# Performance work log

Measured on AMD Instinct MI355X. Metric: run time of the kernel, lower is better.

Reference implementation:

```python
import jax, jax.numpy as jnp
import numpy as np

N = 50000   # nodes
E = 640000  # edges
D_IN = 128
D_OUT = 128
EPS = 1e-5


def _layer_norm(x, gamma, beta):
    mu = jnp.mean(x, axis=-1, keepdims=True)
    var = jnp.mean(jnp.square(x - mu), axis=-1, keepdims=True)
    return (x - mu) * jax.lax.rsqrt(var + EPS) * gamma + beta


def _sage_conv(x, src, dst, w_l, b_l, w_r):
    # PyG SAGEConv (aggr='mean', root_weight=True, normalize=False):
    #   out = lin_l(mean_{j in N(i)} x_j) + lin_r(x_i)
    msgs = x[src]                                             # [E, D]
    agg = jax.ops.segment_sum(msgs, dst, num_segments=N)      # [N, D]
    cnt = jax.ops.segment_sum(jnp.ones((E,), x.dtype), dst, num_segments=N)
    mean = agg / jnp.maximum(cnt, 1.0)[:, None]
    return mean @ w_l.T + b_l + x @ w_r.T


def setup_inputs() -> dict:
    key = jax.random.key(0)
    ks = jax.random.split(key, 12)
    s_in = 1.0 / np.sqrt(D_IN)
    s_out = 1.0 / np.sqrt(D_OUT)
    return {
        "x": jax.random.normal(ks[0], (N, D_IN), jnp.float32),
        "edges": jax.random.randint(ks[1], (2, E), 0, N),
        "dp_w": jax.random.uniform(ks[2], (D_OUT, D_IN), jnp.float32, -s_in, s_in),
        "dp_b": jnp.zeros((D_OUT,), jnp.float32),
        "sc_w": jax.random.uniform(ks[3], (D_OUT, D_IN), jnp.float32, -s_in, s_in),
        "sc_b": jnp.zeros((D_OUT,), jnp.float32),
        "g1_lw": jax.random.uniform(ks[4], (D_OUT, D_OUT), jnp.float32, -s_out, s_out),
        "g1_lb": jnp.zeros((D_OUT,), jnp.float32),
        "g1_rw": jax.random.uniform(ks[5], (D_OUT, D_OUT), jnp.float32, -s_out, s_out),
        "n1_g": jnp.ones((D_OUT,), jnp.float32),
        "n1_b": jnp.zeros((D_OUT,), jnp.float32),
        "g2_lw": jax.random.uniform(ks[6], (D_OUT, D_OUT), jnp.float32, -s_out, s_out),
        "g2_lb": jnp.zeros((D_OUT,), jnp.float32),
        "g2_rw": jax.random.uniform(ks[7], (D_OUT, D_OUT), jnp.float32, -s_out, s_out),
        "n2_g": jnp.ones((D_OUT,), jnp.float32),
        "n2_b": jnp.zeros((D_OUT,), jnp.float32),
    }


def reference(x, edges, dp_w, dp_b, sc_w, sc_b, g1_lw, g1_lb, g1_rw, n1_g, n1_b,
              g2_lw, g2_lb, g2_rw, n2_g, n2_b):
    gelu = lambda v: jax.nn.gelu(v, approximate=False)
    src, dst = edges[0], edges[1]
    shortcut = x @ sc_w.T + sc_b
    h = gelu(x @ dp_w.T + dp_b)
    h = _sage_conv(h, src, dst, g1_lw, g1_lb, g1_rw)
    h = gelu(_layer_norm(h, n1_g, n1_b))
    h = _sage_conv(h, src, dst, g2_lw, g2_lb, g2_rw)
    h = _layer_norm(h, n2_g, n2_b)
    return gelu(h + shortcut)
```

## Files before the change

### kernel.cpp

```cpp
#include <hip/hip_runtime.h>
#include <hip/hip_bf16.h>
#include <math.h>

#define D 128
#define WS 136
#define FS 132
#define PB 128

typedef __attribute__((ext_vector_type(8))) short bf16x8;
typedef __attribute__((ext_vector_type(4))) float f32x4;

__device__ __forceinline__ unsigned short f2bf(float f){
  return (unsigned short)((__float_as_uint(f) + 0x8000u) >> 16);
}
__device__ __forceinline__ float bf2f(unsigned short h){
  return __uint_as_float(((unsigned)h) << 16);
}
__device__ __forceinline__ float bf2f_lo(unsigned v){
  return __uint_as_float(v << 16);
}
__device__ __forceinline__ float bf2f_hi(unsigned v){
  return __uint_as_float(v & 0xFFFF0000u);
}
__device__ __forceinline__ float gelu_fast(float v){
  float u = v * v;
  float arg = v * (1.5957691216f + 0.0713548163f * u);
  arg = fminf(arg, 60.0f);
  float e = __expf(arg);
  return v * e * __builtin_amdgcn_rcpf(e + 1.0f);
}

__global__ __launch_bounds__(256) void k_prepcnt(const float* s0, const float* s1,
    const float* s2, const float* s3, const float* s4, const float* s5,
    unsigned short* dst, const int* __restrict__ edst, int* __restrict__ cnt,
    int E, int nbuck, int epb){
  __shared__ int hist[512];
  if (blockIdx.x < 48){
    int gt = blockIdx.x * 256 + threadIdx.x;
    int m = gt >> 11;
    int r = gt & 2047;
    int f = r >> 6, lane = r & 63;
    int t = f & 7, kk = f >> 3;
    int row = t * 16 + (lane & 15);
    int col = kk * 32 + (lane >> 4) * 8;
    const float* src;
    if (m == 0) src = s0; else if (m == 1) src = s1; else if (m == 2) src = s2;
    else if (m == 3) src = s3; else if (m == 4) src = s4; else src = s5;
    src += row * 128 + col;
    float4 a = *(const float4*)src;
    float4 bb = *(const float4*)(src + 4);
    bf16x8 o;
    o[0] = (short)f2bf(a.x);  o[1] = (short)f2bf(a.y);
    o[2] = (short)f2bf(a.z);  o[3] = (short)f2bf(a.w);
    o[4] = (short)f2bf(bb.x); o[5] = (short)f2bf(bb.y);
    o[6] = (short)f2bf(bb.z); o[7] = (short)f2bf(bb.w);
    int pair = m >> 1, half = m & 1;
    *(bf16x8*)(dst + (size_t)pair * 32768 + (((size_t)f * 2 + half) * 64 + lane) * 8) = o;
    return;
  }
  int blk = blockIdx.x - 48;
  for (int b = threadIdx.x; b < nbuck; b += 256) hist[b] = 0;
  __syncthreads();
  int start = blk * epb;
  int end = min(E, start + epb);
  for (int e = start + threadIdx.x; e < end; e += 256)
    atomicAdd(&hist[edst[e] >> 7], 1);
  __syncthreads();
  for (int b = threadIdx.x; b < nbuck; b += 256) cnt[blk * nbuck + b] = hist[b];
}

__global__ __launch_bounds__(128) void k_scanA(const int* __restrict__ cnt,
    int* __restrict__ offs_rel, int* __restrict__ tot, int nbuck){
  __shared__ int sm[128];
  int b = blockIdx.x, t = threadIdx.x;
  int v = cnt[t * nbuck + b];
  sm[t] = v; __syncthreads();
  for (int ofs = 1; ofs < 128; ofs <<= 1){
    int u = (t >= ofs) ? sm[t - ofs] : 0;
    __syncthreads();
    sm[t] += u;
    __syncthreads();
  }
  offs_rel[t * nbuck + b] = sm[t] - v;
  if (t == 127) tot[b] = sm[127];
}

__global__ __launch_bounds__(256) void k_pscatter(const int* __restrict__ esrc,
    const int* __restrict__ edst, const int* __restrict__ offs_rel,
    const int* __restrict__ tot, unsigned* __restrict__ ebuf,
    int E, int nbuck, int epb){
  __shared__ int stot[512];
  __shared__ int loff[512];
  for (int b = threadIdx.x; b < nbuck; b += 256) stot[b] = tot[b];
  __syncthreads();
  for (int b = threadIdx.x; b < nbuck; b += 256){
    int s = 0;
    for (int j = 0; j < b; j++) s += stot[j];
    loff[b] = s + offs_rel[blockIdx.x * nbuck + b];
  }
  __syncthreads();
  int start = blockIdx.x * epb;
  int end = min(E, start + epb);
  for (int e = start + threadIdx.x; e < end; e += 256){
    int s = esrc[e], d = edst[e];
    int b = d >> 7;
    int pos = atomicAdd(&loff[b], 1);
    ebuf[pos] = (unsigned)s | ((unsigned)(d & 127) << 16);
  }
}

__global__ __launch_bounds__(256) void k_csrin(
    const unsigned* __restrict__ ebuf, const int* __restrict__ tot,
    int* __restrict__ off, int* __restrict__ csr,
    const float* __restrict__ x, const unsigned short* __restrict__ wp,
    const float* __restrict__ scb, const float* __restrict__ dpb,
    unsigned short* __restrict__ sbuf, unsigned short* __restrict__ hbuf,
    int N, int E, int nbuck){
  __shared__ int cnt[128], pref[128], curs[128];
  __shared__ int stot[512], red[256];
  __shared__ unsigned short tile[64 * WS];
  int tid = threadIdx.x;
  if ((int)blockIdx.x < nbuck){
    int b = blockIdx.x;
    for (int j = tid; j < nbuck; j += 256) stot[j] = tot[j];
    __syncthreads();
    int part = 0;
    for (int j = tid; j < b; j += 256) part += stot[j];
    red[tid] = part;
    __syncthreads();
    for (int ofs = 128; ofs > 0; ofs >>= 1){
      if (tid < ofs) red[tid] += red[tid + ofs];
      __syncthreads();
    }
    int start = red[0];
    int end = start + stot[b];
    if (tid < 128) cnt[tid] = 0;
    __syncthreads();
    for (int e = start + tid; e < end; e += 256)
      atomicAdd(&cnt[ebuf[e] >> 16], 1);
    __syncthreads();
    if (tid < 128) pref[tid] = cnt[tid];
    __syncthreads();
    for (int ofs = 1; ofs < 128; ofs <<= 1){
      int v = 0;
      if (tid < 128 && tid >= ofs) v = pref[tid - ofs];
      __syncthreads();
      if (tid < 128) pref[tid] += v;
      __syncthreads();
    }
    if (tid < 128){
      int ex = pref[tid] - cnt[tid];
      curs[tid] = ex;
      int node = b * 128 + tid;
      if (node < N) off[node] = start + ex;
    }
    if (b == 0 && tid == 0) off[N] = E;
    __syncthreads();
    for (int e = start + tid; e < end; e += 256){
      unsigned u = ebuf[e];
      int d = u >> 16;
      int p = atomicAdd(&curs[d], 1);
      csr[start + p] = (int)(u & 0xFFFFu);
    }
    return;
  }
  int bx = blockIdx.x - nbuck;
  int w = tid >> 6, lane = tid & 63, quad = lane >> 4, l16 = lane & 15;
  int nbb = bx * 64;
  int nb = nbb + w * 16;
  int arow = min(nb + l16, N - 1);
  f32x4 acc[2][8];
  #pragma unroll
  for (int m = 0; m < 2; m++)
    #pragma unroll
    for (int t = 0; t < 8; t++) acc[m][t] = (f32x4){0.f, 0.f, 0.f, 0.f};
  #pragma unroll
  for (int kk = 0; kk < 4; kk++){
    const float* xp = x + (size_t)arow * D + kk * 32 + quad * 8;
    float4 xa = *(const float4*)xp;
    float4 xb = *(const float4*)(xp + 4);
    bf16x8 a;
    a[0] = (short)f2bf(xa.x); a[1] = (short)f2bf(xa.y);
    a[2] = (short)f2bf(xa.z); a[3] = (short)f2bf(xa.w);
    a[4] = (short)f2bf(xb.x); a[5] = (short)f2bf(xb.y);
    a[6] = (short)f2bf(xb.z); a[7] = (short)f2bf(xb.w);
    #pragma unroll
    for (int t = 0; t < 8; t++){
      size_t fo = (((size_t)(kk * 8 + t) * 2) * 64 + lane) * 8;
      bf16x8 b0 = *(const bf16x8*)(wp + fo);
      bf16x8 b1 = *(const bf16x8*)(wp + fo + 512);
      acc[0][t] = __builtin_amdgcn_mfma_f32_16x16x32_bf16(a, b0, acc[0][t], 0, 0, 0);
      acc[1][t] = __builtin_amdgcn_mfma_f32_16x16x32_bf16(a, b1, acc[1][t], 0, 0, 0);
    }
  }
  #pragma unroll
  for (int m = 0; m < 2; m++){
    const float* bias = m ? dpb : scb;
    #pragma unroll
    for (int t = 0; t < 8; t++){
      float bv = bias[t * 16 + l16];
      #pragma unroll
      for (int r = 0; r < 4; r++){
        int nl = w * 16 + quad * 4 + r;
        float v = acc[m][t][r] + bv;
        if (m) v = gelu_fast(v);
        tile[nl * WS + t * 16 + l16] = f2bf(v);
      }
    }
    __syncthreads();
    unsigned short* dst = m ? hbuf : sbuf;
    #pragma unroll
    for (int i = 0; i < 4; i++){
      int c = tid + 256 * i;
      int nl = c >> 4, j = c & 15;
      int node = nbb + nl;
      if (node < N)
        *(bf16x8*)(dst + (size_t)node * D + j * 8) = *(const bf16x8*)(tile + nl * WS + j * 8);
    }
    __syncthreads();
  }
}

__global__ __launch_bounds__(256) void k_agg3(const unsigned short* __restrict__ h,
    const int* __restrict__ off, const int* __restrict__ csr,
    unsigned short* __restrict__ mbuf, int N){
  int tid = threadIdx.x;
  int wq = tid >> 4;
  int l16 = tid & 15;
  int n0 = blockIdx.x * 32 + wq * 2;
  if (n0 >= N) return;
  int n1v = (n0 + 1 < N);
  int s0 = off[n0];
  int split = off[n0 + 1];
  int e1 = n1v ? off[n0 + 2] : split;
  float aall[8], ahi[8];
  #pragma unroll
  for (int c = 0; c < 8; c++){ aall[c] = 0.f; ahi[c] = 0.f; }
  if (e1 > s0){
    int nn[8];
    #pragma unroll
    for (int i = 0; i < 8; i++) nn[i] = csr[min(s0 + i, e1 - 1)];
    for (int e = s0; e < e1; e += 8){
      uint4 v[8];
      #pragma unroll
      for (int i = 0; i < 8; i++)
        v[i] = *(const uint4*)(h + (size_t)nn[i] * D + l16 * 8);
      #pragma unroll
      for (int i = 0; i < 8; i++) nn[i] = csr[min(e + 8 + i, e1 - 1)];
      #pragma unroll
      for (int i = 0; i < 8; i++){
        float mv = (e + i < e1) ? 1.f : 0.f;
        float mh = (e + i >= split) ? mv : 0.f;
        aall[0] += mv * bf2f_lo(v[i].x); ahi[0] += mh * bf2f_lo(v[i].x);
        aall[1] += mv * bf2f_hi(v[i].x); ahi[1] += mh * bf2f_hi(v[i].x);
        aall[2] += mv * bf2f_lo(v[i].y); ahi[2] += mh * bf2f_lo(v[i].y);
        aall[3] += mv * bf2f_hi(v[i].y); ahi[3] += mh * bf2f_hi(v[i].y);
        aall[4] += mv * bf2f_lo(v[i].z); ahi[4] += mh * bf2f_lo(v[i].z);
        aall[5] += mv * bf2f_hi(v[i].z); ahi[5] += mh * bf2f_hi(v[i].z);
        aall[6] += mv * bf2f_lo(v[i].w); ahi[6] += mh * bf2f_lo(v[i].w);
        aall[7] += mv * bf2f_hi(v[i].w); ahi[7] += mh * bf2f_hi(v[i].w);
      }
    }
  }
  {
    int deg0 = split - s0;
    float inv = 1.0f / (float)(deg0 > 1 ? deg0 : 1);
    uint4 o;
    o.x = ((unsigned)f2bf((aall[1] - ahi[1]) * inv) << 16) | f2bf((aall[0] - ahi[0]) * inv);
    o.y = ((unsigned)f2bf((aall[3] - ahi[3]) * inv) << 16) | f2bf((aall[2] - ahi[2]) * inv);
    o.z = ((unsigned)f2bf((aall[5] - ahi[5]) * inv) << 16) | f2bf((aall[4] - ahi[4]) * inv);
    o.w = ((unsigned)f2bf((aall[7] - ahi[7]) * inv) << 16) | f2bf((aall[6] - ahi[6]) * inv);
    *(uint4*)(mbuf + (size_t)n0 * D + l16 * 8) = o;
  }
  if (n1v){
    int deg1 = e1 - split;
    float inv = 1.0f / (float)(deg1 > 1 ? deg1 : 1);
    uint4 o;
    o.x = ((unsigned)f2bf(ahi[1] * inv) << 16) | f2bf(ahi[0] * inv);
    o.y = ((unsigned)f2bf(ahi[3] * inv) << 16) | f2bf(ahi[2] * inv);
    o.z = ((unsigned)f2bf(ahi[5] * inv) << 16) | f2bf(ahi[4] * inv);
    o.w = ((unsigned)f2bf(ahi[7] * inv) << 16) | f2bf(ahi[6] * inv);
    *(uint4*)(mbuf + (size_t)(n0 + 1) * D + l16 * 8) = o;
  }
}

__global__ __launch_bounds__(256) void k_g(
    const unsigned short* __restrict__ hin, const unsigned short* __restrict__ mbuf,
    const unsigned short* __restrict__ wp,
    const float* __restrict__ lb, const float* __restrict__ gamma,
    const float* __restrict__ beta,
    const unsigned short* __restrict__ sbuf,
    unsigned short* __restrict__ hout, float* __restrict__ fout, int N, int mode){
  extern __shared__ char smraw[];
  unsigned short* stile = (unsigned short*)smraw;
  float* ftile = (float*)smraw;
  int tid = threadIdx.x, w = tid >> 6, lane = tid & 63, quad = lane >> 4, l16 = lane & 15;
  int nbb = blockIdx.x * 64;
  int nb = nbb + w * 16;
  int arow = min(nb + l16, N - 1);
  f32x4 acc[8];
  #pragma unroll
  for (int t = 0; t < 8; t++) acc[t] = (f32x4){0.f, 0.f, 0.f, 0.f};
  #pragma unroll
  for (int kk = 0; kk < 4; kk++){
    int co = kk * 32 + quad * 8;
    bf16x8 am = *(const bf16x8*)(mbuf + (size_t)arow * D + co);
    bf16x8 ah = *(const bf16x8*)(hin + (size_t)arow * D + co);
    #pragma unroll
    for (int t = 0; t < 8; t++){
      size_t fo = (((size_t)(kk * 8 + t) * 2) * 64 + lane) * 8;
      bf16x8 bl = *(const bf16x8*)(wp + fo);
      bf16x8 br = *(const bf16x8*)(wp + fo + 512);
      acc[t] = __builtin_amdgcn_mfma_f32_16x16x32_bf16(am, bl, acc[t], 0, 0, 0);
      acc[t] = __builtin_amdgcn_mfma_f32_16x16x32_bf16(ah, br, acc[t], 0, 0, 0);
    }
  }
  float lbv[8], gv[8], bv[8];
  #pragma unroll
  for (int t = 0; t < 8; t++){
    lbv[t] = lb[t * 16 + l16];
    gv[t] = gamma[t * 16 + l16];
    bv[t] = beta[t * 16 + l16];
  }
  float mu[4], rs[4];
  #pragma unroll
  for (int r = 0; r < 4; r++){
    float s = 0.f, qq = 0.f;
    #pragma unroll
    for (int t = 0; t < 8; t++){
      float v = acc[t][r] + lbv[t];
      acc[t][r] = v;
      s += v; qq += v * v;
    }
    s += __shfl_xor(s, 1); qq += __shfl_xor(qq, 1);
    s += __shfl_xor(s, 2); qq += __shfl_xor(qq, 2);
    s += __shfl_xor(s, 4); qq += __shfl_xor(qq, 4);
    s += __shfl_xor(s, 8); qq += __shfl_xor(qq, 8);
    float m_ = s * (1.f / 128.f);
    mu[r] = m_;
    rs[r] = rsqrtf(qq * (1.f / 128.f) - m_ * m_ + 1e-5f);
  }
  if (mode == 0){
    #pragma unroll
    for (int t = 0; t < 8; t++)
      #pragma unroll
      for (int r = 0; r < 4; r++){
        int nl = w * 16 + quad * 4 + r;
        float v = (acc[t][r] - mu[r]) * rs[r] * gv[t] + bv[t];
        stile[nl * WS + t * 16 + l16] = f2bf(gelu_fast(v));
      }
    __syncthreads();
    #pragma unroll
    for (int i = 0; i < 4; i++){
      int c = tid + 256 * i;
      int nl = c >> 4, j = c & 15;
      int node = nbb + nl;
      if (node < N)
        *(bf16x8*)(hout + (size_t)node * D + j * 8) = *(const bf16x8*)(stile + nl * WS + j * 8);
    }
  } else {
    #pragma unroll
    for (int i = 0; i < 4; i++){
      int c = tid + 256 * i;
      int nl = c >> 4, j = c & 15;
      int node = nbb + nl;
      bf16x8 v = (bf16x8){0,0,0,0,0,0,0,0};
      if (node < N) v = *(const bf16x8*)(sbuf + (size_t)node * D + j * 8);
      *(bf16x8*)(stile + nl * WS + j * 8) = v;
    }
    __syncthreads();
    float sc[8][4];
    #pragma unroll
    for (int t = 0; t < 8; t++)
      #pragma unroll
      for (int r = 0; r < 4; r++){
        int nl = w * 16 + quad * 4 + r;
        sc[t][r] = bf2f(stile[nl * WS + t * 16 + l16]);
      }
    __syncthreads();
    #pragma unroll
    for (int t = 0; t < 8; t++)
      #pragma unroll
      for (int r = 0; r < 4; r++){
        int nl = w * 16 + quad * 4 + r;
        float v = (acc[t][r] - mu[r]) * rs[r] * gv[t] + bv[t];
        ftile[nl * FS + t * 16 + l16] = gelu_fast(v + sc[t][r]);
      }
    __syncthreads();
    #pragma unroll
    for (int i = 0; i < 8; i++){
      int c = tid + 256 * i;
      int nl = c >> 5, j = c & 31;
      int node = nbb + nl;
      if (node < N)
        *(float4*)(fout + (size_t)node * D + j * 4) = *(const float4*)(ftile + nl * FS + j * 4);
    }
  }
}

extern "C" void kernel_launch(void* const* d_in, const int* in_sizes, int n_in,
                              void* d_out, int out_size, void* d_ws, size_t ws_size,
                              hipStream_t stream){
  const float* x     = (const float*)d_in[0];
  const int*   edges = (const int*)d_in[1];
  const float* dp_w  = (const float*)d_in[2];
  const float* dp_b  = (const float*)d_in[3];
  const float* sc_w  = (const float*)d_in[4];
  const float* sc_b  = (const float*)d_in[5];
  const float* g1_lw = (const float*)d_in[6];
  const float* g1_lb = (const float*)d_in[7];
  const float* g1_rw = (const float*)d_in[8];
  const float* n1_g  = (const float*)d_in[9];
  const float* n1_b  = (const float*)d_in[10];
  const float* g2_lw = (const float*)d_in[11];
  const float* g2_lb = (const float*)d_in[12];
  const float* g2_rw = (const float*)d_in[13];
  const float* n2_g  = (const float*)d_in[14];
  const float* n2_b  = (const float*)d_in[15];

  const int N = in_sizes[0] / D;
  const int E = in_sizes[1] / 2;
  const int* esrc = edges;
  const int* edst = edges + E;
  const int nbuck = (N + 127) >> 7;
  const int epb = (E + PB - 1) / PB;

  char* base = (char*)d_ws;
  size_t cur = 0;
  auto carve = [&](size_t b) -> char* {
    char* p = base + cur;
    cur = (cur + b + 255) & ~(size_t)255;
    return p;
  };
  unsigned* ebuf  = (unsigned*)carve((size_t)E * 4);
  int* cnt        = (int*)carve((size_t)PB * nbuck * 4);
  int* offs_rel   = (int*)carve((size_t)PB * nbuck * 4);
  int* tot        = (int*)carve((size_t)nbuck * 4);
  int* off        = (int*)carve((size_t)(N + 1) * 4);
  int* csr        = (int*)carve((size_t)E * 4);
  unsigned short* wb    = (unsigned short*)carve((size_t)3 * 32768 * 2);
  unsigned short* hbuf  = (unsigned short*)carve((size_t)N * D * 2);
  unsigned short* h1buf = (unsigned short*)carve((size_t)N * D * 2);
  unsigned short* mbuf  = (unsigned short*)carve((size_t)N * D * 2);
  unsigned short* sbuf  = (unsigned short*)carve((size_t)N * D * 2);

  unsigned short* wp0 = wb;
  unsigned short* wp1 = wb + 32768;
  unsigned short* wp2 = wb + 2 * 32768;

  float* out = (float*)d_out;

  k_prepcnt<<<48 + PB, 256, 0, stream>>>(sc_w, dp_w, g1_lw, g1_rw, g2_lw, g2_rw,
                                         wb, edst, cnt, E, nbuck, epb);
  k_scanA<<<nbuck, 128, 0, stream>>>(cnt, offs_rel, tot, nbuck);
  k_pscatter<<<PB, 256, 0, stream>>>(esrc, edst, offs_rel, tot, ebuf, E, nbuck, epb);

  const int nin = (N + 63) / 64;
  k_csrin<<<nbuck + nin, 256, 0, stream>>>(ebuf, tot, off, csr,
                                           x, wp0, sc_b, dp_b, sbuf, hbuf,
                                           N, E, nbuck);

  const int nagg = (N + 31) / 32;
  k_agg3<<<nagg, 256, 0, stream>>>(hbuf, off, csr, mbuf, N);
  k_g<<<nin, 256, 17408, stream>>>(hbuf, mbuf, wp1, g1_lb, n1_g, n1_b,
                                   nullptr, h1buf, nullptr, N, 0);
  k_agg3<<<nagg, 256, 0, stream>>>(h1buf, off, csr, mbuf, N);
  k_g<<<nin, 256, 33792, stream>>>(h1buf, mbuf, wp2, g2_lb, n2_g, n2_b,
                                   sbuf, nullptr, out, N, 1);
}
```

Before: 248.7 us.

## Fuse mean aggregation into SAGE GEMM kernel via shared-memory tile

Merges the CSR neighbor-mean aggregation kernel into the MFMA linear/LayerNorm kernel. Each block now aggregates its 64 nodes, with each 16-lane group handling 4 consecutive nodes through a single prefix-masked sweep over their edges, and writes the bf16 means into shared memory for the GEMM. This removes the global write and re-read of the intermediate mean buffer and two kernel launches. In exchange each thread keeps four sets of accumulators (more registers, possibly lower occupancy), adds a block barrier, and the aggregation now uses the GEMM's grid shape.

```diff
diff --git a/kernel.cpp b/kernel.cpp
--- a/kernel.cpp
+++ b/kernel.cpp
@@ -221,98 +221,104 @@
   }
 }
 
-__global__ __launch_bounds__(256) void k_agg3(const unsigned short* __restrict__ h,
+__global__ __launch_bounds__(256) void k_gall(
+    const unsigned short* __restrict__ hin,
     const int* __restrict__ off, const int* __restrict__ csr,
-    unsigned short* __restrict__ mbuf, int N){
-  int tid = threadIdx.x;
-  int wq = tid >> 4;
-  int l16 = tid & 15;
-  int n0 = blockIdx.x * 32 + wq * 2;
-  if (n0 >= N) return;
-  int n1v = (n0 + 1 < N);
-  int s0 = off[n0];
-  int split = off[n0 + 1];
-  int e1 = n1v ? off[n0 + 2] : split;
-  float aall[8], ahi[8];
-  #pragma unroll
-  for (int c = 0; c < 8; c++){ aall[c] = 0.f; ahi[c] = 0.f; }
-  if (e1 > s0){
-    int nn[8];
-    #pragma unroll
-    for (int i = 0; i < 8; i++) nn[i] = csr[min(s0 + i, e1 - 1)];
-    for (int e = s0; e < e1; e += 8){
-      uint4 v[8];
-      #pragma unroll
-      for (int i = 0; i < 8; i++)
-        v[i] = *(const uint4*)(h + (size_t)nn[i] * D + l16 * 8);
-      #pragma unroll
-      for (int i = 0; i < 8; i++) nn[i] = csr[min(e + 8 + i, e1 - 1)];
-      #pragma unroll
-      for (int i = 0; i < 8; i++){
-        float mv = (e + i < e1) ? 1.f : 0.f;
-        float mh = (e + i >= split) ? mv : 0.f;
-        aall[0] += mv * bf2f_lo(v[i].x); ahi[0] += mh * bf2f_lo(v[i].x);
-        aall[1] += mv * bf2f_hi(v[i].x); ahi[1] += mh * bf2f_hi(v[i].x);
-        aall[2] += mv * bf2f_lo(v[i].y); ahi[2] += mh * bf2f_lo(v[i].y);
-        aall[3] += mv * bf2f_hi(v[i].y); ahi[3] += mh * bf2f_hi(v[i].y);
-        aall[4] += mv * bf2f_lo(v[i].z); ahi[4] += mh * bf2f_lo(v[i].z);
-        aall[5] += mv * bf2f_hi(v[i].z); ahi[5] += mh * bf2f_hi(v[i].z);
-        aall[6] += mv * bf2f_lo(v[i].w); ahi[6] += mh * bf2f_lo(v[i].w);
-        aall[7] += mv * bf2f_hi(v[i].w); ahi[7] += mh * bf2f_hi(v[i].w);
-      }
-    }
-  }
-  {
-    int deg0 = split - s0;
-    float inv = 1.0f / (float)(deg0 > 1 ? deg0 : 1);
-    uint4 o;
-    o.x = ((unsigned)f2bf((aall[1] - ahi[1]) * inv) << 16) | f2bf((aall[0] - ahi[0]) * inv);
-    o.y = ((unsigned)f2bf((aall[3] - ahi[3]) * inv) << 16) | f2bf((aall[2] - ahi[2]) * inv);
-    o.z = ((unsigned)f2bf((aall[5] - ahi[5]) * inv) << 16) | f2bf((aall[4] - ahi[4]) * inv);
-    o.w = ((unsigned)f2bf((aall[7] - ahi[7]) * inv) << 16) | f2bf((aall[6] - ahi[6]) * inv);
-    *(uint4*)(mbuf + (size_t)n0 * D + l16 * 8) = o;
-  }
-  if (n1v){
-    int deg1 = e1 - split;
-    float inv = 1.0f / (float)(deg1 > 1 ? deg1 : 1);
-    uint4 o;
-    o.x = ((unsigned)f2bf(ahi[1] * inv) << 16) | f2bf(ahi[0] * inv);
-    o.y = ((unsigned)f2bf(ahi[3] * inv) << 16) | f2bf(ahi[2] * inv);
-    o.z = ((unsigned)f2bf(ahi[5] * inv) << 16) | f2bf(ahi[4] * inv);
-    o.w = ((unsigned)f2bf(ahi[7] * inv) << 16) | f2bf(ahi[6] * inv);
-    *(uint4*)(mbuf + (size_t)(n0 + 1) * D + l16 * 8) = o;
-  }
-}
-
-__global__ __launch_bounds__(256) void k_g(
-    const unsigned short* __restrict__ hin, const unsigned short* __restrict__ mbuf,
     const unsigned short* __restrict__ wp,
     const float* __restrict__ lb, const float* __restrict__ gamma,
     const float* __restrict__ beta,
     const unsigned short* __restrict__ sbuf,
     unsigned short* __restrict__ hout, float* __restrict__ fout, int N, int mode){
   extern __shared__ char smraw[];
+  unsigned short* mtile = (unsigned short*)smraw;
   unsigned short* stile = (unsigned short*)smraw;
   float* ftile = (float*)smraw;
-  int tid = threadIdx.x, w = tid >> 6, lane = tid & 63, quad = lane >> 4, l16 = lane & 15;
+  int tid = threadIdx.x;
   int nbb = blockIdx.x * 64;
+  {
+    int q = tid >> 4, l16g = tid & 15;
+    int n0 = nbb + q * 4;
+    int s0 = off[min(n0 + 0, N)];
+    int s1 = off[min(n0 + 1, N)];
+    int s2 = off[min(n0 + 2, N)];
+    int s3 = off[min(n0 + 3, N)];
+    int s4 = off[min(n0 + 4, N)];
+    float aT[8], a1[8], a2[8], a3[8];
+    #pragma unroll
+    for (int c = 0; c < 8; c++){ aT[c] = 0.f; a1[c] = 0.f; a2[c] = 0.f; a3[c] = 0.f; }
+    if (s4 > s0){
+      int nn[8];
+      #pragma unroll
+      for (int i = 0; i < 8; i++) nn[i] = csr[min(s0 + i, s4 - 1)];
+      for (int e = s0; e < s4; e += 8){
+        uint4 v[8];
+        #pragma unroll
+        for (int i = 0; i < 8; i++)
+          v[i] = *(const uint4*)(hin + (size_t)nn[i] * D + l16g * 8);
+        #pragma unroll
+        for (int i = 0; i < 8; i++) nn[i] = csr[min(e + 8 + i, s4 - 1)];
+        #pragma unroll
+        for (int i = 0; i < 8; i++){
+          int ei = e + i;
+          float mT = (ei < s4) ? 1.f : 0.f;
+          float m1 = (ei >= s1) ? mT : 0.f;
+          float m2 = (ei >= s2) ? mT : 0.f;
+          float m3 = (ei >= s3) ? mT : 0.f;
+          float fv[8];
+          fv[0] = bf2f_lo(v[i].x); fv[1] = bf2f_hi(v[i].x);
+          fv[2] = bf2f_lo(v[i].y); fv[3] = bf2f_hi(v[i].y);
+          fv[4] = bf2f_lo(v[i].z); fv[5] = bf2f_hi(v[i].z);
+          fv[6] = bf2f_lo(v[i].w); fv[7] = bf2f_hi(v[i].w);
+          #pragma unroll
+          for (int c = 0; c < 8; c++){
+            aT[c] += mT * fv[c];
+            a1[c] += m1 * fv[c];
+            a2[c] += m2 * fv[c];
+            a3[c] += m3 * fv[c];
+          }
+        }
+      }
+    }
+    float i0 = 1.f / (float)max(s1 - s0, 1);
+    float i1 = 1.f / (float)max(s2 - s1, 1);
+    float i2 = 1.f / (float)max(s3 - s2, 1);
+    float i3 = 1.f / (float)max(s4 - s3, 1);
+    bf16x8 o0, o1, o2, o3;
+    #pragma unroll
+    for (int c = 0; c < 8; c++){
+      o0[c] = (short)f2bf((aT[c] - a1[c]) * i0);
+      o1[c] = (short)f2bf((a1[c] - a2[c]) * i1);
+      o2[c] = (short)f2bf((a2[c] - a3[c]) * i2);
+      o3[c] = (short)f2bf(a3[c] * i3);
+    }
+    *(bf16x8*)(mtile + (q * 4 + 0) * WS + l16g * 8) = o0;
+    *(bf16x8*)(mtile + (q * 4 + 1) * WS + l16g * 8) = o1;
+    *(bf16x8*)(mtile + (q * 4 + 2) * WS + l16g * 8) = o2;
+    *(bf16x8*)(mtile + (q * 4 + 3) * WS + l16g * 8) = o3;
+  }
+  __syncthreads();
+  int w = tid >> 6, lane = tid & 63, quad = lane >> 4, l16 = lane & 15;
   int nb = nbb + w * 16;
   int arow = min(nb + l16, N - 1);
+  int mrow = w * 16 + l16;
+  bf16x8 am[4], ah[4];
+  #pragma unroll
+  for (int kk = 0; kk < 4; kk++){
+    am[kk] = *(const bf16x8*)(mtile + mrow * WS + kk * 32 + quad * 8);
+    ah[kk] = *(const bf16x8*)(hin + (size_t)arow * D + kk * 32 + quad * 8);
+  }
   f32x4 acc[8];
   #pragma unroll
   for (int t = 0; t < 8; t++) acc[t] = (f32x4){0.f, 0.f, 0.f, 0.f};
   #pragma unroll
   for (int kk = 0; kk < 4; kk++){
-    int co = kk * 32 + quad * 8;
-    bf16x8 am = *(const bf16x8*)(mbuf + (size_t)arow * D + co);
-    bf16x8 ah = *(const bf16x8*)(hin + (size_t)arow * D + co);
     #pragma unroll
     for (int t = 0; t < 8; t++){
       size_t fo = (((size_t)(kk * 8 + t) * 2) * 64 + lane) * 8;
       bf16x8 bl = *(const bf16x8*)(wp + fo);
       bf16x8 br = *(const bf16x8*)(wp + fo + 512);
-      acc[t] = __builtin_amdgcn_mfma_f32_16x16x32_bf16(am, bl, acc[t], 0, 0, 0);
-      acc[t] = __builtin_amdgcn_mfma_f32_16x16x32_bf16(ah, br, acc[t], 0, 0, 0);
+      acc[t] = __builtin_amdgcn_mfma_f32_16x16x32_bf16(am[kk], bl, acc[t], 0, 0, 0);
+      acc[t] = __builtin_amdgcn_mfma_f32_16x16x32_bf16(ah[kk], br, acc[t], 0, 0, 0);
     }
   }
   float lbv[8], gv[8], bv[8];
@@ -340,6 +346,7 @@
     mu[r] = m_;
     rs[r] = rsqrtf(qq * (1.f / 128.f) - m_ * m_ + 1e-5f);
   }
+  __syncthreads();
   if (mode == 0){
     #pragma unroll
     for (int t = 0; t < 8; t++)
@@ -441,7 +448,6 @@
   unsigned short* wb    = (unsigned short*)carve((size_t)3 * 32768 * 2);
   unsigned short* hbuf  = (unsigned short*)carve((size_t)N * D * 2);
   unsigned short* h1buf = (unsigned short*)carve((size_t)N * D * 2);
-  unsigned short* mbuf  = (unsigned short*)carve((size_t)N * D * 2);
   unsigned short* sbuf  = (unsigned short*)carve((size_t)N * D * 2);
 
   unsigned short* wp0 = wb;
@@ -460,11 +466,8 @@
                                            x, wp0, sc_b, dp_b, sbuf, hbuf,
                                            N, E, nbuck);
 
-  const int nagg = (N + 31) / 32;
-  k_agg3<<<nagg, 256, 0, stream>>>(hbuf, off, csr, mbuf, N);
-  k_g<<<nin, 256, 17408, stream>>>(hbuf, mbuf, wp1, g1_lb, n1_g, n1_b,
-                                   nullptr, h1buf, nullptr, N, 0);
-  k_agg3<<<nagg, 256, 0, stream>>>(h1buf, off, csr, mbuf, N);
-  k_g<<<nin, 256, 33792, stream>>>(h1buf, mbuf, wp2, g2_lb, n2_g, n2_b,
-                                   sbuf, nullptr, out, N, 1);
-}
+  k_gall<<<nin, 256, 17408, stream>>>(hbuf, off, csr, wp1, g1_lb, n1_g, n1_b,
+                                      nullptr, h1buf, nullptr, N, 0);
+  k_gall<<<nin, 256, 33792, stream>>>(h1buf, off, csr, wp2, g2_lb, n2_g, n2_b,
+                                      sbuf, nullptr, out, N, 1);
+}
```

Result: faster. 236.8 us (-4.8%).
